# Optimization experiments

Hardware: AMD Instinct MI355X
Metric: run time of the kernel (lower is better)

## Reference

```python
import jax, jax.numpy as jnp
import numpy as np

B, S, D, H = 64, 2048, 512, 512


def setup_inputs() -> dict:
    key = jax.random.key(0)
    ks = jax.random.split(key, 8)
    return {
        "hidden": jax.random.normal(ks[0], (B, D), dtype=jnp.float32),
        "context": jax.random.normal(ks[1], (B, S, D), dtype=jnp.float32),
        "mask": jax.random.randint(ks[2], (B, S), 0, 2).astype(bool),
        "Wd": jax.random.normal(ks[3], (H, D), dtype=jnp.float32) * 0.05,
        "bd": jax.random.normal(ks[4], (H,), dtype=jnp.float32) * 0.05,
        "We": jax.random.normal(ks[5], (H, D), dtype=jnp.float32) * 0.05,
        "be": jax.random.normal(ks[6], (H,), dtype=jnp.float32) * 0.05,
        "V": jax.random.normal(ks[7], (H,), dtype=jnp.float32) * 0.05,
    }


def reference(hidden, context, mask, Wd, bd, We, be, V):
    # di = d_linear(hidden): [B, H]
    di = hidden @ Wd.T + bd
    # ei = e_linear(context): [B, S, H]
    ei = jnp.einsum("bsd,hd->bsh", context, We) + be
    # additive score u_i = V . tanh(di + ei): [B, S]
    ui = jnp.einsum("h,bsh->bs", V, jnp.tanh(di[:, None, :] + ei))
    # masked positions get -inf (ui[mask] = -inf)
    ui = jnp.where(mask, -jnp.inf, ui)
    alpha = jax.nn.softmax(ui, axis=-1)  # [B, S]
    # context aggregation uses the PROJECTED context ei (as in torch code)
    attention_hidden_state = jnp.einsum("bsh,bs->bh", ei, alpha)
    return alpha, attention_hidden_state
```

## Files before the change

kernel.cpp:

```cpp
#include <hip/hip_runtime.h>
#include <cstdint>

#define B_ 64
#define S_ 2048
#define D_ 512
#define H_ 512

using f32x4  = __attribute__((ext_vector_type(4))) float;
using bf16x8 = __attribute__((ext_vector_type(8))) short;
using u32x2  = __attribute__((ext_vector_type(2))) unsigned int;

__device__ __forceinline__ unsigned short f2bf(float f) {
  unsigned u = __float_as_uint(f);
  u += 0x7FFFu + ((u >> 16) & 1u);
  return (unsigned short)(u >> 16);
}
__device__ __forceinline__ unsigned int cvtpk(float lo, float hi) {
  unsigned int r;
  asm("v_cvt_pk_bf16_f32 %0, %1, %2" : "=v"(r) : "v"(lo), "v"(hi));
  return r;
}
__device__ __forceinline__ float fast_tanh(float x) {
  float t = __builtin_amdgcn_exp2f(x * 2.8853900817779268f);
  return 1.0f - 2.0f * __builtin_amdgcn_rcpf(t + 1.0f);
}

__device__ __forceinline__ void barrier_raw() {
  asm volatile("" ::: "memory");
  __builtin_amdgcn_s_barrier();
  asm volatile("" ::: "memory");
}

__global__ void k_prep(const float* __restrict__ hidden, const float* __restrict__ Wd,
                       const float* __restrict__ bd, float* __restrict__ di,
                       const float* __restrict__ We, unsigned short* __restrict__ Web) {
  if (blockIdx.x < 128) {
    int idx = blockIdx.x * 256 + threadIdx.x;
    int h = idx >> 6;
    int b = idx & 63;
    const f32x4* hp = (const f32x4*)(hidden + (size_t)b * D_);
    const f32x4* wp = (const f32x4*)(Wd + (size_t)h * D_);
    float acc = 0.f;
#pragma unroll 8
    for (int i = 0; i < D_ / 4; ++i) {
      f32x4 x = hp[i], y = wp[i];
      acc += x[0] * y[0] + x[1] * y[1] + x[2] * y[2] + x[3] * y[3];
    }
    di[b * H_ + h] = acc + bd[h];
  } else {
    int i = (blockIdx.x - 128) * 256 + threadIdx.x;
    const f32x4* p = (const f32x4*)(We + (size_t)i * 8);
    f32x4 a = p[0], b = p[1];
    bf16x8 o;
    o[0] = (short)f2bf(a[0]); o[1] = (short)f2bf(a[1]);
    o[2] = (short)f2bf(a[2]); o[3] = (short)f2bf(a[3]);
    o[4] = (short)f2bf(b[0]); o[5] = (short)f2bf(b[1]);
    o[6] = (short)f2bf(b[2]); o[7] = (short)f2bf(b[3]);
    *(bf16x8*)(Web + (size_t)i * 8) = o;
  }
}

__global__ __launch_bounds__(256, 3) void k_ei_gemm(
    const float* __restrict__ A, const unsigned short* __restrict__ Bw,
    const float* __restrict__ be, const float* __restrict__ V,
    const float* __restrict__ di, float* __restrict__ ui4) {
  __shared__ __align__(16) unsigned short ldsA[2][128 * 32];
  __shared__ __align__(16) unsigned short ldsB[2][128 * 32];
  __shared__ float ured[4][64];

  const int bid = blockIdx.x;
  const int swz = (bid & 7) * 512 + (bid >> 3);
  const int row0 = (swz >> 2) << 7;
  const int nt   = swz & 3;
  const int col0 = nt << 7;

  const int t  = threadIdx.x;
  const int l  = t & 63;
  const int w  = t >> 6;
  const int wm = (w >> 1) << 6;
  const int wn = (w & 1) << 6;
  const int lr = l & 15;
  const int lg = l >> 4;

  const float* gA = A + (size_t)(row0 + w * 32 + (l >> 3)) * D_ + ((l & 7) << 2);
  const unsigned short* gB = Bw + (size_t)(col0 + w * 32 + (l >> 2)) * D_ + ((l & 3) << 3);

  const int sA = (((l & 7) >> 1) ^ ((l >> 4) & 3));
  const int eA0 = (w * 32 + (l >> 3)) * 32 + sA * 8 + (l & 1) * 4;
  const int sB = ((l & 3) ^ ((l >> 3) & 3));
  const int eB0 = (w * 32 + (l >> 2)) * 32 + sB * 8;

  const int rs = (lg ^ ((lr >> 1) & 3)) << 3;

  f32x4  rA0, rA1, rA2, rA3;
  bf16x8 rB0, rB1;

#define LOAD(kk) do {                                   \
    const float* a_ = gA + ((kk) << 5);                 \
    rA0 = *(const f32x4*)(a_);                          \
    rA1 = *(const f32x4*)(a_ + 8 * D_);                 \
    rA2 = *(const f32x4*)(a_ + 16 * D_);                \
    rA3 = *(const f32x4*)(a_ + 24 * D_);                \
    const unsigned short* b_ = gB + ((kk) << 5);        \
    rB0 = *(const bf16x8*)(b_);                         \
    rB1 = *(const bf16x8*)(b_ + 16 * D_);               \
  } while (0)

#define WRITE(bf) do {                                                  \
    u32x2 p0 = {cvtpk(rA0[0], rA0[1]), cvtpk(rA0[2], rA0[3])};          \
    u32x2 p1 = {cvtpk(rA1[0], rA1[1]), cvtpk(rA1[2], rA1[3])};          \
    u32x2 p2 = {cvtpk(rA2[0], rA2[1]), cvtpk(rA2[2], rA2[3])};          \
    u32x2 p3 = {cvtpk(rA3[0], rA3[1]), cvtpk(rA3[2], rA3[3])};          \
    *(u32x2*)&ldsA[bf][eA0]       = p0;                                 \
    *(u32x2*)&ldsA[bf][eA0 + 256] = p1;                                 \
    *(u32x2*)&ldsA[bf][eA0 + 512] = p2;                                 \
    *(u32x2*)&ldsA[bf][eA0 + 768] = p3;                                 \
    *(bf16x8*)&ldsB[bf][eB0]       = rB0;                               \
    *(bf16x8*)&ldsB[bf][eB0 + 512] = rB1;                               \
  } while (0)

  f32x4 acc[4][4];
  const f32x4 z = {0.f, 0.f, 0.f, 0.f};
#pragma unroll
  for (int mi = 0; mi < 4; ++mi)
#pragma unroll
    for (int ni = 0; ni < 4; ++ni) acc[mi][ni] = z;

  LOAD(0);
  WRITE(0);
  LOAD(1);

  for (int kt = 0; kt < 16; ++kt) {
    const int bf = kt & 1;
    asm volatile("s_waitcnt lgkmcnt(0)" ::: "memory");
    barrier_raw();

    bf16x8 af[4], bq[4];
#pragma unroll
    for (int mi = 0; mi < 4; ++mi)
      af[mi] = *(const bf16x8*)&ldsA[bf][(wm + mi * 16 + lr) * 32 + rs];
#pragma unroll
    for (int ni = 0; ni < 4; ++ni)
      bq[ni] = *(const bf16x8*)&ldsB[bf][(wn + ni * 16 + lr) * 32 + rs];

    if (kt + 1 < 16) WRITE(bf ^ 1);
    if (kt + 2 < 16) LOAD(kt + 2);

    __builtin_amdgcn_s_setprio(1);
#pragma unroll
    for (int mi = 0; mi < 4; ++mi)
#pragma unroll
      for (int ni = 0; ni < 4; ++ni)
        acc[mi][ni] = __builtin_amdgcn_mfma_f32_16x16x32_bf16(
            af[mi], bq[ni], acc[mi][ni], 0, 0, 0);
    __builtin_amdgcn_s_setprio(0);
  }
#undef LOAD
#undef WRITE

  const int b = row0 >> 11;
  float uacc[4][4];
#pragma unroll
  for (int mi = 0; mi < 4; ++mi)
#pragma unroll
    for (int j = 0; j < 4; ++j) uacc[mi][j] = 0.f;

#pragma unroll
  for (int ni = 0; ni < 4; ++ni) {
    const int gc = col0 + wn + ni * 16 + lr;
    const float vv = V[gc];
    const float base = di[b * H_ + gc] + be[gc];
#pragma unroll
    for (int mi = 0; mi < 4; ++mi)
#pragma unroll
      for (int j = 0; j < 4; ++j)
        uacc[mi][j] += vv * fast_tanh(base + acc[mi][ni][j]);
  }
#pragma unroll
  for (int mi = 0; mi < 4; ++mi)
#pragma unroll
    for (int j = 0; j < 4; ++j) {
      float s = uacc[mi][j];
      s += __shfl_xor(s, 1);
      s += __shfl_xor(s, 2);
      s += __shfl_xor(s, 4);
      s += __shfl_xor(s, 8);
      if (lr == 0) ured[w][mi * 16 + (lg << 2) + j] = s;
    }
  __syncthreads();
  if (t < 128) {
    const int r = t & 63, half = t >> 6;
    ui4[nt * (B_ * S_) + row0 + half * 64 + r] =
        ured[half * 2][r] + ured[half * 2 + 1][r];
  }
}

__global__ void k_softmax(const float* __restrict__ ui4, const void* __restrict__ mask,
                          float* __restrict__ alpha) {
  __shared__ float red[4];
  __shared__ int sfl;
  const int b = blockIdx.x, t = threadIdx.x;
  const int l = t & 63, w = t >> 6;

  if (t == 0) sfl = 0;
  const unsigned int* mw = (const unsigned int*)mask;
  unsigned det = (mw[b * 512 + t] | mw[b * 512 + 256 + t]) & 0xFFFFFF00u;
  __syncthreads();
  if (det) atomicOr(&sfl, 1);
  __syncthreads();
  const int fl = sfl;

  float u[8];
#pragma unroll
  for (int i = 0; i < 8; ++i) {
    const int idx = b * S_ + t + i * 256;
    const int msk = fl ? (int)((const unsigned char*)mask)[idx]
                       : ((const int*)mask)[idx];
    const float uv = ui4[idx] + ui4[idx + B_ * S_] + ui4[idx + 2 * B_ * S_] +
                     ui4[idx + 3 * B_ * S_];
    u[i] = msk ? -__builtin_inff() : uv;
  }

  float mx = u[0];
#pragma unroll
  for (int i = 1; i < 8; ++i) mx = fmaxf(mx, u[i]);
#pragma unroll
  for (int off = 32; off; off >>= 1) mx = fmaxf(mx, __shfl_xor(mx, off));
  if (l == 0) red[w] = mx;
  __syncthreads();
  mx = fmaxf(fmaxf(red[0], red[1]), fmaxf(red[2], red[3]));
  __syncthreads();

  float p[8];
  float s = 0.f;
#pragma unroll
  for (int i = 0; i < 8; ++i) {
    p[i] = __builtin_amdgcn_exp2f((u[i] - mx) * 1.4426950408889634f);
    s += p[i];
  }
#pragma unroll
  for (int off = 32; off; off >>= 1) s += __shfl_xor(s, off);
  if (l == 0) red[w] = s;
  __syncthreads();
  s = red[0] + red[1] + red[2] + red[3];

  const float inv = 1.0f / s;
#pragma unroll
  for (int i = 0; i < 8; ++i) alpha[b * S_ + t + i * 256] = p[i] * inv;
}

__global__ void k_wsum(const float* __restrict__ ctx, const float* __restrict__ alpha,
                       float* __restrict__ part) {
  __shared__ float red[3][512];
  const int b = blockIdx.x >> 4, chunk = blockIdx.x & 15;
  const int t = threadIdx.x;
  const int h0 = (t & 63) << 3;
  const int sw = t >> 6;
  const int s0 = chunk << 7;

  float acc[8] = {0.f, 0.f, 0.f, 0.f, 0.f, 0.f, 0.f, 0.f};
#pragma unroll 2
  for (int k = 0; k < 32; ++k) {
    const int s = s0 + sw + (k << 2);
    const float a = alpha[b * S_ + s];
    const f32x4* e = (const f32x4*)(ctx + ((size_t)(b * S_ + s)) * D_ + h0);
    f32x4 e0 = e[0], e1 = e[1];
#pragma unroll
    for (int j = 0; j < 4; ++j) acc[j] += a * e0[j];
#pragma unroll
    for (int j = 0; j < 4; ++j) acc[4 + j] += a * e1[j];
  }
  if (sw) {
#pragma unroll
    for (int j = 0; j < 8; ++j) red[sw - 1][h0 + j] = acc[j];
  }
  __syncthreads();
  if (sw == 0) {
#pragma unroll
    for (int j = 0; j < 8; ++j)
      part[((chunk << 6) + b) * 512 + h0 + j] =
          acc[j] + red[0][h0 + j] + red[1][h0 + j] + red[2][h0 + j];
  }
}

__global__ void k_tail(const float* __restrict__ part, const float* __restrict__ We,
                       const float* __restrict__ be, float* __restrict__ out1) {
  __shared__ float wsum_s[512];
  const int b = blockIdx.x, t = threadIdx.x;

  float s = 0.f;
#pragma unroll
  for (int c = 0; c < 16; ++c) s += part[((c << 6) + b) * 512 + t];
  wsum_s[t] = s;
  __syncthreads();

  const f32x4* wp = (const f32x4*)wsum_s;
  const f32x4* ep = (const f32x4*)(We + (size_t)t * D_);
  float acc = 0.f;
#pragma unroll 8
  for (int i = 0; i < D_ / 4; ++i) {
    f32x4 x = wp[i], y = ep[i];
    acc += x[0] * y[0] + x[1] * y[1] + x[2] * y[2] + x[3] * y[3];
  }
  out1[b * H_ + t] = acc + be[t];
}

extern "C" void kernel_launch(void* const* d_in, const int* in_sizes, int n_in,
                              void* d_out, int out_size, void* d_ws, size_t ws_size,
                              hipStream_t stream) {
  const float* hidden = (const float*)d_in[0];
  const float* ctx    = (const float*)d_in[1];
  const void*  mask   = d_in[2];
  const float* Wd     = (const float*)d_in[3];
  const float* bd     = (const float*)d_in[4];
  const float* We     = (const float*)d_in[5];
  const float* be     = (const float*)d_in[6];
  const float* V      = (const float*)d_in[7];

  float* out   = (float*)d_out;
  float* alpha = out;
  float* out1  = out + B_ * S_;

  char* ws = (char*)d_ws;
  const size_t off_u2  = 0;
  const size_t off_r3  = off_u2 + 4ull * B_ * S_ * 4;
  const size_t off_web = off_r3 + (size_t)B_ * H_ * 4;

  float* ui4  = (float*)(ws + off_u2);
  float* part = (float*)(ws + off_u2);
  float* di   = (float*)(ws + off_r3);
  unsigned short* Web = (unsigned short*)(ws + off_web);

  k_prep<<<256, 256, 0, stream>>>(hidden, Wd, bd, di, We, Web);
  k_ei_gemm<<<(B_ * S_ / 128) * 4, 256, 0, stream>>>(ctx, Web, be, V, di, ui4);
  k_softmax<<<B_, 256, 0, stream>>>(ui4, mask, alpha);
  k_wsum<<<B_ * 16, 256, 0, stream>>>(ctx, alpha, part);
  k_tail<<<B_, 512, 0, stream>>>(part, We, be, out1);
}
```

Measured before the change: 208.3 us.

## Double-buffer global-load registers and move the LDS write after the MFMAs

The main K loop is unrolled by two and uses two register sets for the staged global tiles. The global load for step kt+2 is now issued before the MFMA block. The bf16 conversion and LDS write of the next tile happen after the MFMAs instead of before them. This gives global loads a full iteration to land and keeps MFMA issue from waiting on the convert and store. The cost is higher VGPR pressure from the second set of staging registers, which could lower occupancy.

```diff
diff --git a/kernel.cpp b/kernel.cpp
--- a/kernel.cpp
+++ b/kernel.cpp
@@ -92,31 +92,31 @@
 
   const int rs = (lg ^ ((lr >> 1) & 3)) << 3;
 
-  f32x4  rA0, rA1, rA2, rA3;
-  bf16x8 rB0, rB1;
-
-#define LOAD(kk) do {                                   \
+  f32x4  rA0a, rA1a, rA2a, rA3a;  bf16x8 rB0a, rB1a;
+  f32x4  rA0b, rA1b, rA2b, rA3b;  bf16x8 rB0b, rB1b;
+
+#define LOADN(S, kk) do {                               \
     const float* a_ = gA + ((kk) << 5);                 \
-    rA0 = *(const f32x4*)(a_);                          \
-    rA1 = *(const f32x4*)(a_ + 8 * D_);                 \
-    rA2 = *(const f32x4*)(a_ + 16 * D_);                \
-    rA3 = *(const f32x4*)(a_ + 24 * D_);                \
+    rA0##S = *(const f32x4*)(a_);                       \
+    rA1##S = *(const f32x4*)(a_ + 8 * D_);              \
+    rA2##S = *(const f32x4*)(a_ + 16 * D_);             \
+    rA3##S = *(const f32x4*)(a_ + 24 * D_);             \
     const unsigned short* b_ = gB + ((kk) << 5);        \
-    rB0 = *(const bf16x8*)(b_);                         \
-    rB1 = *(const bf16x8*)(b_ + 16 * D_);               \
+    rB0##S = *(const bf16x8*)(b_);                      \
+    rB1##S = *(const bf16x8*)(b_ + 16 * D_);            \
   } while (0)
 
-#define WRITE(bf) do {                                                  \
-    u32x2 p0 = {cvtpk(rA0[0], rA0[1]), cvtpk(rA0[2], rA0[3])};          \
-    u32x2 p1 = {cvtpk(rA1[0], rA1[1]), cvtpk(rA1[2], rA1[3])};          \
-    u32x2 p2 = {cvtpk(rA2[0], rA2[1]), cvtpk(rA2[2], rA2[3])};          \
-    u32x2 p3 = {cvtpk(rA3[0], rA3[1]), cvtpk(rA3[2], rA3[3])};          \
-    *(u32x2*)&ldsA[bf][eA0]       = p0;                                 \
-    *(u32x2*)&ldsA[bf][eA0 + 256] = p1;                                 \
-    *(u32x2*)&ldsA[bf][eA0 + 512] = p2;                                 \
-    *(u32x2*)&ldsA[bf][eA0 + 768] = p3;                                 \
-    *(bf16x8*)&ldsB[bf][eB0]       = rB0;                               \
-    *(bf16x8*)&ldsB[bf][eB0 + 512] = rB1;                               \
+#define WRITEN(S, bf) do {                                                  \
+    u32x2 p0 = {cvtpk(rA0##S[0], rA0##S[1]), cvtpk(rA0##S[2], rA0##S[3])};  \
+    u32x2 p1 = {cvtpk(rA1##S[0], rA1##S[1]), cvtpk(rA1##S[2], rA1##S[3])};  \
+    u32x2 p2 = {cvtpk(rA2##S[0], rA2##S[1]), cvtpk(rA2##S[2], rA2##S[3])};  \
+    u32x2 p3 = {cvtpk(rA3##S[0], rA3##S[1]), cvtpk(rA3##S[2], rA3##S[3])};  \
+    *(u32x2*)&ldsA[bf][eA0]       = p0;                                     \
+    *(u32x2*)&ldsA[bf][eA0 + 256] = p1;                                     \
+    *(u32x2*)&ldsA[bf][eA0 + 512] = p2;                                     \
+    *(u32x2*)&ldsA[bf][eA0 + 768] = p3;                                     \
+    *(bf16x8*)&ldsB[bf][eB0]       = rB0##S;                                \
+    *(bf16x8*)&ldsB[bf][eB0 + 512] = rB1##S;                                \
   } while (0)
 
   f32x4 acc[4][4];
@@ -126,37 +126,38 @@
 #pragma unroll
     for (int ni = 0; ni < 4; ++ni) acc[mi][ni] = z;
 
-  LOAD(0);
-  WRITE(0);
-  LOAD(1);
-
-  for (int kt = 0; kt < 16; ++kt) {
-    const int bf = kt & 1;
-    asm volatile("s_waitcnt lgkmcnt(0)" ::: "memory");
-    barrier_raw();
-
-    bf16x8 af[4], bq[4];
-#pragma unroll
-    for (int mi = 0; mi < 4; ++mi)
-      af[mi] = *(const bf16x8*)&ldsA[bf][(wm + mi * 16 + lr) * 32 + rs];
-#pragma unroll
-    for (int ni = 0; ni < 4; ++ni)
-      bq[ni] = *(const bf16x8*)&ldsB[bf][(wn + ni * 16 + lr) * 32 + rs];
-
-    if (kt + 1 < 16) WRITE(bf ^ 1);
-    if (kt + 2 < 16) LOAD(kt + 2);
-
-    __builtin_amdgcn_s_setprio(1);
-#pragma unroll
-    for (int mi = 0; mi < 4; ++mi)
-#pragma unroll
-      for (int ni = 0; ni < 4; ++ni)
-        acc[mi][ni] = __builtin_amdgcn_mfma_f32_16x16x32_bf16(
-            af[mi], bq[ni], acc[mi][ni], 0, 0, 0);
-    __builtin_amdgcn_s_setprio(0);
-  }
-#undef LOAD
-#undef WRITE
+#define KBODY(bf, LD, WR) do {                                              \
+    asm volatile("s_waitcnt lgkmcnt(0)" ::: "memory");                      \
+    barrier_raw();                                                          \
+    bf16x8 af[4], bq[4];                                                    \
+    _Pragma("unroll") for (int mi = 0; mi < 4; ++mi)                        \
+      af[mi] = *(const bf16x8*)&ldsA[bf][(wm + mi * 16 + lr) * 32 + rs];    \
+    _Pragma("unroll") for (int ni = 0; ni < 4; ++ni)                        \
+      bq[ni] = *(const bf16x8*)&ldsB[bf][(wn + ni * 16 + lr) * 32 + rs];    \
+    LD;                                                                     \
+    __builtin_amdgcn_s_setprio(1);                                          \
+    _Pragma("unroll") for (int mi = 0; mi < 4; ++mi)                        \
+      _Pragma("unroll") for (int ni = 0; ni < 4; ++ni)                      \
+        acc[mi][ni] = __builtin_amdgcn_mfma_f32_16x16x32_bf16(              \
+            af[mi], bq[ni], acc[mi][ni], 0, 0, 0);                          \
+    __builtin_amdgcn_s_setprio(0);                                          \
+    WR;                                                                     \
+  } while (0)
+
+  LOADN(a, 0);
+  WRITEN(a, 0);
+  LOADN(b, 1);
+
+  for (int u = 0; u < 7; ++u) {
+    const int kt = 2 * u;
+    KBODY(0, LOADN(a, kt + 2), WRITEN(b, 1));
+    KBODY(1, LOADN(b, kt + 3), WRITEN(a, 0));
+  }
+  KBODY(0, (void)0, WRITEN(b, 1));
+  KBODY(1, (void)0, (void)0);
+#undef KBODY
+#undef LOADN
+#undef WRITEN
 
   const int b = row0 >> 11;
   float uacc[4][4];
```

Measured after the change: 201.8 us. 3.1% less time.

## Stage GEMM tiles via direct global-to-LDS loads with wider 128x256 tiles

Applied to the files above, without the earlier changes.

The ei GEMM now copies fp32 context and bf16 weight tiles straight from global memory into LDS with global_load_lds, instead of going through registers. The fp32 to bf16 conversion moves to after the LDS read, and the XOR swizzle is applied on the global addresses. The block grows to 512 threads covering 256 output columns, which halves how often the context is re-read across column tiles and halves the partial-score buffer the softmax has to sum. The cost is twice the LDS footprint for A (it is stored as fp32), conversion work repeated in every wave, and lower occupancy.

```diff
diff --git a/kernel.cpp b/kernel.cpp
--- a/kernel.cpp
+++ b/kernel.cpp
@@ -8,7 +8,6 @@
 
 using f32x4  = __attribute__((ext_vector_type(4))) float;
 using bf16x8 = __attribute__((ext_vector_type(8))) short;
-using u32x2  = __attribute__((ext_vector_type(2))) unsigned int;
 
 __device__ __forceinline__ unsigned short f2bf(float f) {
   unsigned u = __float_as_uint(f);
@@ -20,9 +19,21 @@
   asm("v_cvt_pk_bf16_f32 %0, %1, %2" : "=v"(r) : "v"(lo), "v"(hi));
   return r;
 }
+__device__ __forceinline__ bf16x8 cvt8(f32x4 a, f32x4 b) {
+  union { unsigned int u[4]; bf16x8 v; } r;
+  r.u[0] = cvtpk(a[0], a[1]); r.u[1] = cvtpk(a[2], a[3]);
+  r.u[2] = cvtpk(b[0], b[1]); r.u[3] = cvtpk(b[2], b[3]);
+  return r.v;
+}
 __device__ __forceinline__ float fast_tanh(float x) {
   float t = __builtin_amdgcn_exp2f(x * 2.8853900817779268f);
   return 1.0f - 2.0f * __builtin_amdgcn_rcpf(t + 1.0f);
+}
+
+__device__ __forceinline__ void gl_lds16g(const void* g, void* l) {
+  __builtin_amdgcn_global_load_lds(
+      (const __attribute__((address_space(1))) unsigned int*)g,
+      (__attribute__((address_space(3))) unsigned int*)l, 16, 0, 0);
 }
 
 __device__ __forceinline__ void barrier_raw() {
@@ -60,64 +71,46 @@
   }
 }
 
-__global__ __launch_bounds__(256, 3) void k_ei_gemm(
+__global__ __launch_bounds__(512, 2) void k_ei_gemm(
     const float* __restrict__ A, const unsigned short* __restrict__ Bw,
     const float* __restrict__ be, const float* __restrict__ V,
-    const float* __restrict__ di, float* __restrict__ ui4) {
-  __shared__ __align__(16) unsigned short ldsA[2][128 * 32];
-  __shared__ __align__(16) unsigned short ldsB[2][128 * 32];
-  __shared__ float ured[4][64];
+    const float* __restrict__ di, float* __restrict__ ui2) {
+  __shared__ __align__(16) float ldsA[2][128 * 32];
+  __shared__ __align__(16) unsigned short ldsB[2][256 * 32];
+  __shared__ float ured[8][64];
 
   const int bid = blockIdx.x;
-  const int swz = (bid & 7) * 512 + (bid >> 3);
-  const int row0 = (swz >> 2) << 7;
-  const int nt   = swz & 3;
-  const int col0 = nt << 7;
+  const int swz = (bid & 7) * 256 + (bid >> 3);
+  const int row0 = (swz >> 1) << 7;
+  const int nt   = swz & 1;
+  const int cb   = nt << 8;
 
   const int t  = threadIdx.x;
   const int l  = t & 63;
   const int w  = t >> 6;
-  const int wm = (w >> 1) << 6;
-  const int wn = (w & 1) << 6;
+  const int wm = (w >> 2) << 6;
+  const int wn = (w & 3) << 6;
   const int lr = l & 15;
   const int lg = l >> 4;
 
-  const float* gA = A + (size_t)(row0 + w * 32 + (l >> 3)) * D_ + ((l & 7) << 2);
-  const unsigned short* gB = Bw + (size_t)(col0 + w * 32 + (l >> 2)) * D_ + ((l & 3) << 3);
-
-  const int sA = (((l & 7) >> 1) ^ ((l >> 4) & 3));
-  const int eA0 = (w * 32 + (l >> 3)) * 32 + sA * 8 + (l & 1) * 4;
-  const int sB = ((l & 3) ^ ((l >> 3) & 3));
-  const int eB0 = (w * 32 + (l >> 2)) * 32 + sB * 8;
-
-  const int rs = (lg ^ ((lr >> 1) & 3)) << 3;
-
-  f32x4  rA0, rA1, rA2, rA3;
-  bf16x8 rB0, rB1;
-
-#define LOAD(kk) do {                                   \
-    const float* a_ = gA + ((kk) << 5);                 \
-    rA0 = *(const f32x4*)(a_);                          \
-    rA1 = *(const f32x4*)(a_ + 8 * D_);                 \
-    rA2 = *(const f32x4*)(a_ + 16 * D_);                \
-    rA3 = *(const f32x4*)(a_ + 24 * D_);                \
-    const unsigned short* b_ = gB + ((kk) << 5);        \
-    rB0 = *(const bf16x8*)(b_);                         \
-    rB1 = *(const bf16x8*)(b_ + 16 * D_);               \
+  const float* gA = A + (size_t)(row0 + w * 8 + (l >> 3)) * D_ +
+                    (((l & 7) ^ ((l >> 3) & 7)) << 2);
+  const unsigned short* gB = Bw + (size_t)(cb + w * 16 + (l >> 2)) * D_ +
+                             (((l & 3) ^ ((l >> 3) & 3)) << 3);
+
+#define STAGE(bf, kk) do {                                     \
+    const int k0_ = (kk) << 5;                                 \
+    gl_lds16g(gA + k0_,            &ldsA[bf][w * 256]);        \
+    gl_lds16g(gA + 64 * D_ + k0_,  &ldsA[bf][2048 + w * 256]); \
+    gl_lds16g(gB + k0_,            &ldsB[bf][w * 512]);        \
+    gl_lds16g(gB + 128 * D_ + k0_, &ldsB[bf][4096 + w * 512]); \
   } while (0)
 
-#define WRITE(bf) do {                                                  \
-    u32x2 p0 = {cvtpk(rA0[0], rA0[1]), cvtpk(rA0[2], rA0[3])};          \
-    u32x2 p1 = {cvtpk(rA1[0], rA1[1]), cvtpk(rA1[2], rA1[3])};          \
-    u32x2 p2 = {cvtpk(rA2[0], rA2[1]), cvtpk(rA2[2], rA2[3])};          \
-    u32x2 p3 = {cvtpk(rA3[0], rA3[1]), cvtpk(rA3[2], rA3[3])};          \
-    *(u32x2*)&ldsA[bf][eA0]       = p0;                                 \
-    *(u32x2*)&ldsA[bf][eA0 + 256] = p1;                                 \
-    *(u32x2*)&ldsA[bf][eA0 + 512] = p2;                                 \
-    *(u32x2*)&ldsA[bf][eA0 + 768] = p3;                                 \
-    *(bf16x8*)&ldsB[bf][eB0]       = rB0;                               \
-    *(bf16x8*)&ldsB[bf][eB0 + 512] = rB1;                               \
-  } while (0)
+  const int pa0 = (((2 * lg)     ^ (lr & 7)) << 2);
+  const int pa1 = (((2 * lg + 1) ^ (lr & 7)) << 2);
+  const int rsB = (lg ^ ((lr >> 1) & 3)) << 3;
+  const int arow = (wm + lr) * 32;
+  const int brow = (wn + lr) * 32;
 
   f32x4 acc[4][4];
   const f32x4 z = {0.f, 0.f, 0.f, 0.f};
@@ -126,37 +119,61 @@
 #pragma unroll
     for (int ni = 0; ni < 4; ++ni) acc[mi][ni] = z;
 
-  LOAD(0);
-  WRITE(0);
-  LOAD(1);
-
+  STAGE(0, 0);
+  STAGE(1, 1);
+
+#pragma unroll
   for (int kt = 0; kt < 16; ++kt) {
+    if (kt == 15) asm volatile("s_waitcnt vmcnt(0)" ::: "memory");
+    else          asm volatile("s_waitcnt vmcnt(4)" ::: "memory");
+    barrier_raw();
     const int bf = kt & 1;
-    asm volatile("s_waitcnt lgkmcnt(0)" ::: "memory");
+
+    bf16x8 bq0 = *(const bf16x8*)&ldsB[bf][brow + 0 * 512 + rsB];
+    bf16x8 bq1 = *(const bf16x8*)&ldsB[bf][brow + 1 * 512 + rsB];
+    bf16x8 bq2 = *(const bf16x8*)&ldsB[bf][brow + 2 * 512 + rsB];
+    bf16x8 bq3 = *(const bf16x8*)&ldsB[bf][brow + 3 * 512 + rsB];
+
+    __builtin_amdgcn_s_setprio(1);
+    {
+      f32x4 r00 = *(const f32x4*)&ldsA[bf][arow + 0 * 512 + pa0];
+      f32x4 r01 = *(const f32x4*)&ldsA[bf][arow + 0 * 512 + pa1];
+      f32x4 r10 = *(const f32x4*)&ldsA[bf][arow + 1 * 512 + pa0];
+      f32x4 r11 = *(const f32x4*)&ldsA[bf][arow + 1 * 512 + pa1];
+      bf16x8 af0 = cvt8(r00, r01);
+      bf16x8 af1 = cvt8(r10, r11);
+      acc[0][0] = __builtin_amdgcn_mfma_f32_16x16x32_bf16(af0, bq0, acc[0][0], 0, 0, 0);
+      acc[0][1] = __builtin_amdgcn_mfma_f32_16x16x32_bf16(af0, bq1, acc[0][1], 0, 0, 0);
+      acc[0][2] = __builtin_amdgcn_mfma_f32_16x16x32_bf16(af0, bq2, acc[0][2], 0, 0, 0);
+      acc[0][3] = __builtin_amdgcn_mfma_f32_16x16x32_bf16(af0, bq3, acc[0][3], 0, 0, 0);
+      acc[1][0] = __builtin_amdgcn_mfma_f32_16x16x32_bf16(af1, bq0, acc[1][0], 0, 0, 0);
+      acc[1][1] = __builtin_amdgcn_mfma_f32_16x16x32_bf16(af1, bq1, acc[1][1], 0, 0, 0);
+      acc[1][2] = __builtin_amdgcn_mfma_f32_16x16x32_bf16(af1, bq2, acc[1][2], 0, 0, 0);
+      acc[1][3] = __builtin_amdgcn_mfma_f32_16x16x32_bf16(af1, bq3, acc[1][3], 0, 0, 0);
+    }
+    {
+      f32x4 r20 = *(const f32x4*)&ldsA[bf][arow + 2 * 512 + pa0];
+      f32x4 r21 = *(const f32x4*)&ldsA[bf][arow + 2 * 512 + pa1];
+      f32x4 r30 = *(const f32x4*)&ldsA[bf][arow + 3 * 512 + pa0];
+      f32x4 r31 = *(const f32x4*)&ldsA[bf][arow + 3 * 512 + pa1];
+      bf16x8 af2 = cvt8(r20, r21);
+      bf16x8 af3 = cvt8(r30, r31);
+      acc[2][0] = __builtin_amdgcn_mfma_f32_16x16x32_bf16(af2, bq0, acc[2][0], 0, 0, 0);
+      acc[2][1] = __builtin_amdgcn_mfma_f32_16x16x32_bf16(af2, bq1, acc[2][1], 0, 0, 0);
+      acc[2][2] = __builtin_amdgcn_mfma_f32_16x16x32_bf16(af2, bq2, acc[2][2], 0, 0, 0);
+      acc[2][3] = __builtin_amdgcn_mfma_f32_16x16x32_bf16(af2, bq3, acc[2][3], 0, 0, 0);
+      acc[3][0] = __builtin_amdgcn_mfma_f32_16x16x32_bf16(af3, bq0, acc[3][0], 0, 0, 0);
+      acc[3][1] = __builtin_amdgcn_mfma_f32_16x16x32_bf16(af3, bq1, acc[3][1], 0, 0, 0);
+      acc[3][2] = __builtin_amdgcn_mfma_f32_16x16x32_bf16(af3, bq2, acc[3][2], 0, 0, 0);
+      acc[3][3] = __builtin_amdgcn_mfma_f32_16x16x32_bf16(af3, bq3, acc[3][3], 0, 0, 0);
+    }
+    __builtin_amdgcn_s_setprio(0);
+
+    __builtin_amdgcn_sched_barrier(0);
     barrier_raw();
-
-    bf16x8 af[4], bq[4];
-#pragma unroll
-    for (int mi = 0; mi < 4; ++mi)
-      af[mi] = *(const bf16x8*)&ldsA[bf][(wm + mi * 16 + lr) * 32 + rs];
-#pragma unroll
-    for (int ni = 0; ni < 4; ++ni)
-      bq[ni] = *(const bf16x8*)&ldsB[bf][(wn + ni * 16 + lr) * 32 + rs];
-
-    if (kt + 1 < 16) WRITE(bf ^ 1);
-    if (kt + 2 < 16) LOAD(kt + 2);
-
-    __builtin_amdgcn_s_setprio(1);
-#pragma unroll
-    for (int mi = 0; mi < 4; ++mi)
-#pragma unroll
-      for (int ni = 0; ni < 4; ++ni)
-        acc[mi][ni] = __builtin_amdgcn_mfma_f32_16x16x32_bf16(
-            af[mi], bq[ni], acc[mi][ni], 0, 0, 0);
-    __builtin_amdgcn_s_setprio(0);
-  }
-#undef LOAD
-#undef WRITE
+    if (kt + 2 < 16) STAGE(bf, kt + 2);
+  }
+#undef STAGE
 
   const int b = row0 >> 11;
   float uacc[4][4];
@@ -167,7 +184,7 @@
 
 #pragma unroll
   for (int ni = 0; ni < 4; ++ni) {
-    const int gc = col0 + wn + ni * 16 + lr;
+    const int gc = cb + wn + ni * 16 + lr;
     const float vv = V[gc];
     const float base = di[b * H_ + gc] + be[gc];
 #pragma unroll
@@ -189,13 +206,14 @@
     }
   __syncthreads();
   if (t < 128) {
-    const int r = t & 63, half = t >> 6;
-    ui4[nt * (B_ * S_) + row0 + half * 64 + r] =
-        ured[half * 2][r] + ured[half * 2 + 1][r];
-  }
-}
-
-__global__ void k_softmax(const float* __restrict__ ui4, const void* __restrict__ mask,
+    const int r = t & 63, wr = t >> 6;
+    ui2[nt * (B_ * S_) + row0 + wr * 64 + r] =
+        ured[wr * 4][r] + ured[wr * 4 + 1][r] + ured[wr * 4 + 2][r] +
+        ured[wr * 4 + 3][r];
+  }
+}
+
+__global__ void k_softmax(const float* __restrict__ ui2, const void* __restrict__ mask,
                           float* __restrict__ alpha) {
   __shared__ float red[4];
   __shared__ int sfl;
@@ -216,8 +234,7 @@
     const int idx = b * S_ + t + i * 256;
     const int msk = fl ? (int)((const unsigned char*)mask)[idx]
                        : ((const int*)mask)[idx];
-    const float uv = ui4[idx] + ui4[idx + B_ * S_] + ui4[idx + 2 * B_ * S_] +
-                     ui4[idx + 3 * B_ * S_];
+    const float uv = ui2[idx] + ui2[idx + B_ * S_];
     u[i] = msk ? -__builtin_inff() : uv;
   }
 
@@ -326,14 +343,14 @@
   const size_t off_r3  = off_u2 + 4ull * B_ * S_ * 4;
   const size_t off_web = off_r3 + (size_t)B_ * H_ * 4;
 
-  float* ui4  = (float*)(ws + off_u2);
+  float* ui2  = (float*)(ws + off_u2);
   float* part = (float*)(ws + off_u2);
   float* di   = (float*)(ws + off_r3);
   unsigned short* Web = (unsigned short*)(ws + off_web);
 
   k_prep<<<256, 256, 0, stream>>>(hidden, Wd, bd, di, We, Web);
-  k_ei_gemm<<<(B_ * S_ / 128) * 4, 256, 0, stream>>>(ctx, Web, be, V, di, ui4);
-  k_softmax<<<B_, 256, 0, stream>>>(ui4, mask, alpha);
+  k_ei_gemm<<<(B_ * S_ / 128) * 2, 512, 0, stream>>>(ctx, Web, be, V, di, ui2);
+  k_softmax<<<B_, 256, 0, stream>>>(ui2, mask, alpha);
   k_wsum<<<B_ * 16, 256, 0, stream>>>(ctx, alpha, part);
   k_tail<<<B_, 512, 0, stream>>>(part, We, be, out1);
 }
```

After: 205.4 us. No clear change (-1.4%).

## Give each GEMM block the full H width and DMA We tiles into LDS

Applied to the files above, without the earlier changes.

The ei GEMM now computes 64 context rows against all 512 hidden columns per 512-thread block. Before, it computed 128x128 tiles split into four column slices. This reads each context row once instead of four times and writes one ui value per row, so the four-way partial buffer and its reduction in softmax go away. The bf16 We tiles are loaded straight into LDS with global_load_lds, using explicit vmcnt waits and an extra barrier. The trade-offs are much more We traffic per block (512x32 per k-step), fewer resident blocks (launch bounds 512,1), and a second barrier in every iteration.

```diff
diff --git a/kernel.cpp b/kernel.cpp
--- a/kernel.cpp
+++ b/kernel.cpp
@@ -23,6 +23,12 @@
 __device__ __forceinline__ float fast_tanh(float x) {
   float t = __builtin_amdgcn_exp2f(x * 2.8853900817779268f);
   return 1.0f - 2.0f * __builtin_amdgcn_rcpf(t + 1.0f);
+}
+
+__device__ __forceinline__ void gl_lds16g(const void* g, void* l) {
+  __builtin_amdgcn_global_load_lds(
+      (const __attribute__((address_space(1))) unsigned int*)g,
+      (__attribute__((address_space(3))) unsigned int*)l, 16, 0, 0);
 }
 
 __device__ __forceinline__ void barrier_raw() {
@@ -60,63 +66,44 @@
   }
 }
 
-__global__ __launch_bounds__(256, 3) void k_ei_gemm(
+__global__ __launch_bounds__(512, 1) void k_ei_gemm(
     const float* __restrict__ A, const unsigned short* __restrict__ Bw,
     const float* __restrict__ be, const float* __restrict__ V,
-    const float* __restrict__ di, float* __restrict__ ui4) {
-  __shared__ __align__(16) unsigned short ldsA[2][128 * 32];
-  __shared__ __align__(16) unsigned short ldsB[2][128 * 32];
-  __shared__ float ured[4][64];
+    const float* __restrict__ di, float* __restrict__ ui) {
+  __shared__ __align__(16) unsigned short ldsA[2][64 * 32];
+  __shared__ __align__(16) unsigned short ldsB[2][512 * 32];
+  __shared__ float ured[8][64];
 
   const int bid = blockIdx.x;
-  const int swz = (bid & 7) * 512 + (bid >> 3);
-  const int row0 = (swz >> 2) << 7;
-  const int nt   = swz & 3;
-  const int col0 = nt << 7;
+  const int row0 = bid << 6;
 
   const int t  = threadIdx.x;
   const int l  = t & 63;
   const int w  = t >> 6;
-  const int wm = (w >> 1) << 6;
-  const int wn = (w & 1) << 6;
+  const int wn = w << 6;
   const int lr = l & 15;
   const int lg = l >> 4;
 
-  const float* gA = A + (size_t)(row0 + w * 32 + (l >> 3)) * D_ + ((l & 7) << 2);
-  const unsigned short* gB = Bw + (size_t)(col0 + w * 32 + (l >> 2)) * D_ + ((l & 3) << 3);
-
-  const int sA = (((l & 7) >> 1) ^ ((l >> 4) & 3));
-  const int eA0 = (w * 32 + (l >> 3)) * 32 + sA * 8 + (l & 1) * 4;
-  const int sB = ((l & 3) ^ ((l >> 3) & 3));
-  const int eB0 = (w * 32 + (l >> 2)) * 32 + sB * 8;
-
-  const int rs = (lg ^ ((lr >> 1) & 3)) << 3;
-
-  f32x4  rA0, rA1, rA2, rA3;
-  bf16x8 rB0, rB1;
-
-#define LOAD(kk) do {                                   \
-    const float* a_ = gA + ((kk) << 5);                 \
-    rA0 = *(const f32x4*)(a_);                          \
-    rA1 = *(const f32x4*)(a_ + 8 * D_);                 \
-    rA2 = *(const f32x4*)(a_ + 16 * D_);                \
-    rA3 = *(const f32x4*)(a_ + 24 * D_);                \
-    const unsigned short* b_ = gB + ((kk) << 5);        \
-    rB0 = *(const bf16x8*)(b_);                         \
-    rB1 = *(const bf16x8*)(b_ + 16 * D_);               \
+  const float* gA = A + (size_t)(row0 + (t >> 3)) * D_ + ((t & 7) << 2);
+  const int eAslot = (((t >> 1) & 3) ^ ((t >> 3) & 3) ^ ((t >> 5) & 3));
+  const int eA = (t >> 3) * 32 + eAslot * 8 + (t & 1) * 4;
+  const int segr = (l >> 2);
+  const int srcg = ((l & 3) ^ ((l >> 2) & 3) ^ ((l >> 4) & 3));
+  const int rs = ((lg ^ (lr & 3) ^ ((lr >> 2) & 3)) << 3);
+
+  f32x4 areg;
+
+#define LOADA(kt) do { areg = *(const f32x4*)(gA + ((kt) << 5)); } while (0)
+#define WRITEA(bf) do {                                             \
+    u32x2 p_ = {cvtpk(areg[0], areg[1]), cvtpk(areg[2], areg[3])};  \
+    *(u32x2*)&ldsA[bf][eA] = p_;                                    \
   } while (0)
-
-#define WRITE(bf) do {                                                  \
-    u32x2 p0 = {cvtpk(rA0[0], rA0[1]), cvtpk(rA0[2], rA0[3])};          \
-    u32x2 p1 = {cvtpk(rA1[0], rA1[1]), cvtpk(rA1[2], rA1[3])};          \
-    u32x2 p2 = {cvtpk(rA2[0], rA2[1]), cvtpk(rA2[2], rA2[3])};          \
-    u32x2 p3 = {cvtpk(rA3[0], rA3[1]), cvtpk(rA3[2], rA3[3])};          \
-    *(u32x2*)&ldsA[bf][eA0]       = p0;                                 \
-    *(u32x2*)&ldsA[bf][eA0 + 256] = p1;                                 \
-    *(u32x2*)&ldsA[bf][eA0 + 512] = p2;                                 \
-    *(u32x2*)&ldsA[bf][eA0 + 768] = p3;                                 \
-    *(bf16x8*)&ldsB[bf][eB0]       = rB0;                               \
-    *(bf16x8*)&ldsB[bf][eB0 + 512] = rB1;                               \
+#define DMAB(bf, kt) do {                                                      \
+    _Pragma("unroll") for (int d_ = 0; d_ < 4; ++d_) {                         \
+      const int s_ = w * 4 + d_;                                               \
+      gl_lds16g(Bw + (size_t)(s_ * 16 + segr) * D_ + ((kt) << 5) + srcg * 8,   \
+                &ldsB[bf][(s_ * 16) * 32]);                                    \
+    }                                                                          \
   } while (0)
 
   f32x4 acc[4][4];
@@ -126,25 +113,30 @@
 #pragma unroll
     for (int ni = 0; ni < 4; ++ni) acc[mi][ni] = z;
 
-  LOAD(0);
-  WRITE(0);
-  LOAD(1);
+  LOADA(0);
+  DMAB(0, 0);
+  WRITEA(0);
+  LOADA(1);
+  DMAB(1, 1);
 
   for (int kt = 0; kt < 16; ++kt) {
+    if (kt < 15)
+      asm volatile("s_waitcnt vmcnt(5) lgkmcnt(0)" ::: "memory");
+    else
+      asm volatile("s_waitcnt vmcnt(0) lgkmcnt(0)" ::: "memory");
+    barrier_raw();
     const int bf = kt & 1;
-    asm volatile("s_waitcnt lgkmcnt(0)" ::: "memory");
-    barrier_raw();
 
     bf16x8 af[4], bq[4];
 #pragma unroll
     for (int mi = 0; mi < 4; ++mi)
-      af[mi] = *(const bf16x8*)&ldsA[bf][(wm + mi * 16 + lr) * 32 + rs];
+      af[mi] = *(const bf16x8*)&ldsA[bf][(mi * 16 + lr) * 32 + rs];
 #pragma unroll
     for (int ni = 0; ni < 4; ++ni)
       bq[ni] = *(const bf16x8*)&ldsB[bf][(wn + ni * 16 + lr) * 32 + rs];
 
-    if (kt + 1 < 16) WRITE(bf ^ 1);
-    if (kt + 2 < 16) LOAD(kt + 2);
+    if (kt < 15) WRITEA(bf ^ 1);
+    if (kt < 14) LOADA(kt + 2);
 
     __builtin_amdgcn_s_setprio(1);
 #pragma unroll
@@ -154,9 +146,13 @@
         acc[mi][ni] = __builtin_amdgcn_mfma_f32_16x16x32_bf16(
             af[mi], bq[ni], acc[mi][ni], 0, 0, 0);
     __builtin_amdgcn_s_setprio(0);
-  }
-#undef LOAD
-#undef WRITE
+
+    barrier_raw();
+    if (kt < 14) DMAB(bf, kt + 2);
+  }
+#undef LOADA
+#undef WRITEA
+#undef DMAB
 
   const int b = row0 >> 11;
   float uacc[4][4];
@@ -167,7 +163,7 @@
 
 #pragma unroll
   for (int ni = 0; ni < 4; ++ni) {
-    const int gc = col0 + wn + ni * 16 + lr;
+    const int gc = wn + ni * 16 + lr;
     const float vv = V[gc];
     const float base = di[b * H_ + gc] + be[gc];
 #pragma unroll
@@ -188,14 +184,15 @@
       if (lr == 0) ured[w][mi * 16 + (lg << 2) + j] = s;
     }
   __syncthreads();
-  if (t < 128) {
-    const int r = t & 63, half = t >> 6;
-    ui4[nt * (B_ * S_) + row0 + half * 64 + r] =
-        ured[half * 2][r] + ured[half * 2 + 1][r];
-  }
-}
-
-__global__ void k_softmax(const float* __restrict__ ui4, const void* __restrict__ mask,
+  if (t < 64) {
+    float s = 0.f;
+#pragma unroll
+    for (int ww = 0; ww < 8; ++ww) s += ured[ww][t];
+    ui[row0 + t] = s;
+  }
+}
+
+__global__ void k_softmax(const float* __restrict__ ui, const void* __restrict__ mask,
                           float* __restrict__ alpha) {
   __shared__ float red[4];
   __shared__ int sfl;
@@ -216,9 +213,7 @@
     const int idx = b * S_ + t + i * 256;
     const int msk = fl ? (int)((const unsigned char*)mask)[idx]
                        : ((const int*)mask)[idx];
-    const float uv = ui4[idx] + ui4[idx + B_ * S_] + ui4[idx + 2 * B_ * S_] +
-                     ui4[idx + 3 * B_ * S_];
-    u[i] = msk ? -__builtin_inff() : uv;
+    u[i] = msk ? -__builtin_inff() : ui[idx];
   }
 
   float mx = u[0];
@@ -322,18 +317,19 @@
   float* out1  = out + B_ * S_;
 
   char* ws = (char*)d_ws;
-  const size_t off_u2  = 0;
-  const size_t off_r3  = off_u2 + 4ull * B_ * S_ * 4;
-  const size_t off_web = off_r3 + (size_t)B_ * H_ * 4;
-
-  float* ui4  = (float*)(ws + off_u2);
-  float* part = (float*)(ws + off_u2);
-  float* di   = (float*)(ws + off_r3);
+  const size_t off_ui   = 0;
+  const size_t off_part = off_ui + (size_t)B_ * S_ * 4;
+  const size_t off_di   = off_part + 16ull * B_ * D_ * 4;
+  const size_t off_web  = off_di + (size_t)B_ * H_ * 4;
+
+  float* ui   = (float*)(ws + off_ui);
+  float* part = (float*)(ws + off_part);
+  float* di   = (float*)(ws + off_di);
   unsigned short* Web = (unsigned short*)(ws + off_web);
 
   k_prep<<<256, 256, 0, stream>>>(hidden, Wd, bd, di, We, Web);
-  k_ei_gemm<<<(B_ * S_ / 128) * 4, 256, 0, stream>>>(ctx, Web, be, V, di, ui4);
-  k_softmax<<<B_, 256, 0, stream>>>(ui4, mask, alpha);
+  k_ei_gemm<<<B_ * S_ / 64, 512, 0, stream>>>(ctx, Web, be, V, di, ui);
+  k_softmax<<<B_, 256, 0, stream>>>(ui, mask, alpha);
   k_wsum<<<B_ * 16, 256, 0, stream>>>(ctx, alpha, part);
   k_tail<<<B_, 512, 0, stream>>>(part, We, be, out1);
 }
```

Result: slower. 272.4 us (+30.8%).
